# Kernel tuning notes

Measured on AMD Instinct MI355X. Metric: run time of the kernel, lower is better.

The kernel has to match this reference:

```python
import jax, jax.numpy as jnp
import numpy as np

N = 50000
E = 800000
IN_DIM = 128
OUT_DIM = 128
EDGE_DIM = 3
H = 4
HD = OUT_DIM // H  # 32
SCALE = HD ** -0.5


def setup_inputs() -> dict:
    key = jax.random.key(0)
    ks = jax.random.split(key, 10)
    x = jax.random.normal(ks[0], (N, IN_DIM), dtype=jnp.float32)
    edge_index = jax.random.randint(ks[1], (2, E), 0, N, dtype=jnp.int64)
    edge_attr = jax.random.normal(ks[2], (E, EDGE_DIM), dtype=jnp.float32)
    s = 1.0 / np.sqrt(IN_DIM)
    Wq = jax.random.normal(ks[3], (IN_DIM, H * HD), dtype=jnp.float32) * s
    Wk = jax.random.normal(ks[4], (IN_DIM, H * HD), dtype=jnp.float32) * s
    Wv = jax.random.normal(ks[5], (IN_DIM, H * HD), dtype=jnp.float32) * s
    We = jax.random.normal(ks[6], (EDGE_DIM, H), dtype=jnp.float32) * (1.0 / np.sqrt(EDGE_DIM))
    Wo = jax.random.normal(ks[7], (H * HD, OUT_DIM), dtype=jnp.float32) * (1.0 / np.sqrt(H * HD))
    bo = jnp.zeros((OUT_DIM,), dtype=jnp.float32)
    Wm = jax.random.normal(ks[8], (IN_DIM + OUT_DIM, OUT_DIM), dtype=jnp.float32) * (1.0 / np.sqrt(IN_DIM + OUT_DIM))
    bm = jnp.zeros((OUT_DIM,), dtype=jnp.float32)
    return {"x": x, "edge_index": edge_index, "edge_attr": edge_attr,
            "Wq": Wq, "Wk": Wk, "Wv": Wv, "We": We, "Wo": Wo, "bo": bo,
            "Wm": Wm, "bm": bm}


def reference(x, edge_index, edge_attr, Wq, Wk, Wv, We, Wo, bo, Wm, bm):
    n = x.shape[0]
    src = edge_index[0]
    dst = edge_index[1]
    Q = (x @ Wq).reshape(n, H, HD)
    K = (x @ Wk).reshape(n, H, HD)
    V = (x @ Wv).reshape(n, H, HD)
    edge_bias = edge_attr @ We                                  # [E, H]
    attn = jnp.sum(Q[dst] * K[src], axis=-1) * SCALE + edge_bias  # [E, H]
    attn = jnp.where(attn >= 0, attn, 0.2 * attn)               # leaky_relu(0.2)
    # NOTE: original uses a single GLOBAL max over all edges/heads for stability
    attn_exp = jnp.exp(attn - jnp.max(attn))
    attn_sum = jax.ops.segment_sum(attn_exp, dst, num_segments=n)  # [N, H]
    attn_norm = attn_exp / jnp.maximum(attn_sum[dst], 1e-12)
    # dropout disabled (eval mode)
    weighted_V = V[src] * attn_norm[:, :, None]                 # [E, H, HD]
    agg = jax.ops.segment_sum(weighted_V, dst, num_segments=n)  # [N, H, HD]
    agg = agg.reshape(n, H * HD) @ Wo + bo                      # [N, OUT]
    h = jnp.concatenate([x, agg], axis=1) @ Wm + bm
    return jax.nn.relu(h)
```

## Files before the change

kernel.cpp:

```cpp
#include <hip/hip_runtime.h>
#include <hip/hip_bf16.h>
#include <math.h>

#define NN 50000
#define NE 800000
#define DIM 128
#define NH 4
#define HD 32
#define EH (NE * NH)
#define ATTN_SCALE 0.17677669529663687f
#define MTILE 64
#define GEMM_BLOCKS 782
#define NBKT 98
#define PTS 2048
#define PBLKS 391
#define HBLKS 104

typedef unsigned int uint;
typedef unsigned short ushort;
typedef __attribute__((ext_vector_type(8))) short short8;
typedef __attribute__((ext_vector_type(4))) float f32x4;

__device__ inline ushort f2bf(float f) {
    __hip_bfloat16 h = __float2bfloat16(f);
    return *(ushort*)&h;
}
__device__ inline float bflo(uint u) { return __uint_as_float(u << 16); }
__device__ inline float bfhi(uint u) { return __uint_as_float(u & 0xffff0000u); }

__global__ __launch_bounds__(256) void prep_x_kernel(
    const float* __restrict__ x, ushort* __restrict__ xb)
{
    const int i = blockIdx.x * 256 + threadIdx.x;
    const float4 v = ((const float4*)x)[i];
    ushort4 o;
    o.x = f2bf(v.x); o.y = f2bf(v.y); o.z = f2bf(v.z); o.w = f2bf(v.w);
    ((ushort4*)xb)[i] = o;
}

__global__ __launch_bounds__(128) void prep_wx_kernel(
    const float* __restrict__ Wo, const float* __restrict__ Wm,
    float* __restrict__ Wx)
{
    const int r = blockIdx.x, j = threadIdx.x;
    float acc = 0.f;
    for (int t = 0; t < 128; ++t)
        acc = fmaf(Wo[r * 128 + t], Wm[(128 + t) * 128 + j], acc);
    Wx[r * 128 + j] = acc;
}

__global__ __launch_bounds__(128) void prep_bias_kernel(
    const float* __restrict__ bo, const float* __restrict__ bm,
    const float* __restrict__ Wm, float* __restrict__ bprime)
{
    const int j = threadIdx.x;
    float acc = bm[j];
    for (int t = 0; t < 128; ++t)
        acc = fmaf(bo[t], Wm[(128 + t) * 128 + j], acc);
    bprime[j] = acc;
}

__global__ __launch_bounds__(256) void pack_qkv_kernel(
    const float* __restrict__ Wq, const float* __restrict__ Wk,
    const float* __restrict__ Wv, short* __restrict__ Bp)
{
    const int idx = blockIdx.x * 256 + threadIdx.x;
    const int j = idx & 7, lane = (idx >> 3) & 63;
    const int rest = idx >> 9;
    const int nt = rest % 24, kc = rest / 24;
    const int k = kc * 32 + (lane >> 4) * 8 + j;
    const int n = nt * 16 + (lane & 15);
    const float* W = (n < 128) ? Wq : (n < 256 ? Wk : Wv);
    Bp[idx] = (short)f2bf(W[k * 128 + (n & 127)]);
}

__global__ __launch_bounds__(256) void pack_out_kernel(
    const float* __restrict__ Wm, const float* __restrict__ Wx,
    short* __restrict__ Bp)
{
    const int idx = blockIdx.x * 256 + threadIdx.x;
    const int j = idx & 7, lane = (idx >> 3) & 63;
    const int rest = idx >> 9;
    const int nt = rest & 7, kc = rest >> 3;
    const int k = kc * 32 + (lane >> 4) * 8 + j;
    const int n = nt * 16 + (lane & 15);
    const float v = (k < 128) ? Wm[k * 128 + n] : Wx[(k - 128) * 128 + n];
    Bp[idx] = (short)f2bf(v);
}

__global__ __launch_bounds__(128) void bkt_zero_kernel(int* __restrict__ bkt_cnt)
{
    if (threadIdx.x < 128) bkt_cnt[threadIdx.x] = 0;
}

__global__ __launch_bounds__(256) void bkt_hist_kernel(
    const int* __restrict__ dst, int* __restrict__ bkt_cnt)
{
    __shared__ int c[NBKT];
    const int tid = threadIdx.x;
    if (tid < NBKT) c[tid] = 0;
    __syncthreads();
    for (int e = blockIdx.x * 256 + tid; e < NE; e += HBLKS * 256)
        atomicAdd(&c[dst[e] >> 9], 1);
    __syncthreads();
    if (tid < NBKT && c[tid]) atomicAdd(&bkt_cnt[tid], c[tid]);
}

__global__ void bkt_scan_kernel(const int* __restrict__ bkt_cnt,
                                int* __restrict__ bkt_base,
                                int* __restrict__ bkt_cursor,
                                int* __restrict__ rowptr)
{
    if (threadIdx.x == 0) {
        int run = 0;
        for (int b = 0; b < NBKT; ++b) {
            bkt_base[b] = run;
            bkt_cursor[b] = run;
            run += bkt_cnt[b];
        }
        bkt_base[NBKT] = run;
        rowptr[NN] = run;
    }
}

__global__ __launch_bounds__(256) void partition_kernel(
    const int* __restrict__ src, const int* __restrict__ dst,
    const float* __restrict__ edge_attr, const float* __restrict__ We,
    int* __restrict__ bkt_cursor,
    int* __restrict__ psrc, int* __restrict__ pdst, float* __restrict__ peb)
{
    __shared__ int cnt[NBKT], rbase[NBKT], cnt2[NBKT];
    const int tid = threadIdx.x;
    if (tid < NBKT) cnt[tid] = 0;
    __syncthreads();
    const int e0 = blockIdx.x * PTS;
    #pragma unroll
    for (int it = 0; it < 8; ++it) {
        const int e = e0 + it * 256 + tid;
        if (e < NE) atomicAdd(&cnt[dst[e] >> 9], 1);
    }
    __syncthreads();
    if (tid < NBKT) {
        rbase[tid] = cnt[tid] ? atomicAdd(&bkt_cursor[tid], cnt[tid]) : 0;
        cnt2[tid] = 0;
    }
    __syncthreads();
    #pragma unroll
    for (int it = 0; it < 8; ++it) {
        const int e = e0 + it * 256 + tid;
        if (e < NE) {
            const int d = dst[e];
            const int b = d >> 9;
            const int r = atomicAdd(&cnt2[b], 1);
            const int pos = rbase[b] + r;
            psrc[pos] = src[e];
            pdst[pos] = d;
            const float a0 = edge_attr[e * 3 + 0];
            const float a1 = edge_attr[e * 3 + 1];
            const float a2 = edge_attr[e * 3 + 2];
            float4 eb;
            eb.x = a0 * We[0] + a1 * We[4] + a2 * We[8];
            eb.y = a0 * We[1] + a1 * We[5] + a2 * We[9];
            eb.z = a0 * We[2] + a1 * We[6] + a2 * We[10];
            eb.w = a0 * We[3] + a1 * We[7] + a2 * We[11];
            *(float4*)(peb + (size_t)pos * 4) = eb;
        }
    }
}

__global__ __launch_bounds__(256) void bucket_csr_kernel(
    const int* __restrict__ bkt_base,
    const int* __restrict__ psrc, const int* __restrict__ pdst,
    const float* __restrict__ peb,
    int* __restrict__ rowptr,
    int* __restrict__ srcp, float* __restrict__ eb_csr)
{
    __shared__ int cnt[512];
    __shared__ int pre[512];
    __shared__ int sc[256];
    const int tid = threadIdx.x;
    const int b = blockIdx.x;
    const int base = bkt_base[b];
    const int n = bkt_base[b + 1] - base;
    const int node0 = b << 9;

    cnt[tid] = 0; cnt[tid + 256] = 0;
    __syncthreads();
    for (int i = base + tid; i < base + n; i += 256)
        atomicAdd(&cnt[pdst[i] - node0], 1);
    __syncthreads();

    const int pair = cnt[2 * tid] + cnt[2 * tid + 1];
    sc[tid] = pair;
    __syncthreads();
    for (int off = 1; off < 256; off <<= 1) {
        const int v = (tid >= off) ? sc[tid - off] : 0;
        __syncthreads();
        sc[tid] += v;
        __syncthreads();
    }
    const int ex = sc[tid] - pair;
    pre[2 * tid] = base + ex;
    pre[2 * tid + 1] = base + ex + cnt[2 * tid];
    __syncthreads();

    for (int l = tid; l < 512; l += 256) {
        const int g = node0 + l;
        if (g < NN) rowptr[g] = pre[l];
    }
    __syncthreads();

    for (int i = base + tid; i < base + n; i += 256) {
        const int d = pdst[i];
        const int pos = atomicAdd(&pre[d - node0], 1);
        srcp[pos] = psrc[i];
        *(float4*)(eb_csr + (size_t)pos * 4) =
            *(const float4*)(peb + (size_t)i * 4);
    }
}

__global__ __launch_bounds__(256) void qkv_mfma_kernel(
    const ushort* __restrict__ xb, const short* __restrict__ Bp,
    ushort* __restrict__ Qb, ushort* __restrict__ Kb, ushort* __restrict__ Vb)
{
    const int wave = threadIdx.x >> 6;
    const int lane = threadIdx.x & 63;
    const int m = lane & 15, quad = lane >> 4;
    const int row0w = blockIdx.x * MTILE + wave * 16;
    const int arow = row0w + m;
    const bool rowok = arow < NN;

    short8 a[4];
    #pragma unroll
    for (int kc = 0; kc < 4; ++kc)
        a[kc] = rowok ? *(const short8*)(xb + (size_t)arow * 128 + kc * 32 + quad * 8)
                      : (short8)(0);

    const int NT = 24;
    for (int nt = 0; nt < NT; nt += 2) {
        f32x4 acc0 = {0.f, 0.f, 0.f, 0.f}, acc1 = {0.f, 0.f, 0.f, 0.f};
        #pragma unroll
        for (int kc = 0; kc < 4; ++kc) {
            const short8 b0 = *(const short8*)(Bp + ((size_t)(kc * NT + nt) * 64 + lane) * 8);
            const short8 b1 = *(const short8*)(Bp + ((size_t)(kc * NT + nt + 1) * 64 + lane) * 8);
            acc0 = __builtin_amdgcn_mfma_f32_16x16x32_bf16(a[kc], b0, acc0, 0, 0, 0);
            acc1 = __builtin_amdgcn_mfma_f32_16x16x32_bf16(a[kc], b1, acc1, 0, 0, 0);
        }
        #pragma unroll
        for (int t = 0; t < 2; ++t) {
            const f32x4 acc = t ? acc1 : acc0;
            const int c = (nt + t) * 16 + m;
            ushort* dstp_ = (c < 128) ? Qb : (c < 256 ? Kb : Vb);
            const int lc = c & 127;
            #pragma unroll
            for (int g = 0; g < 4; ++g) {
                const int r = row0w + quad * 4 + g;
                if (r < NN) dstp_[(size_t)r * 128 + lc] = f2bf(acc[g]);
            }
        }
    }
}

__global__ __launch_bounds__(256) void out_mfma_kernel(
    const ushort* __restrict__ xb, const ushort* __restrict__ aggb,
    const short* __restrict__ Bp, const float* __restrict__ bprime,
    float* __restrict__ out)
{
    const int wave = threadIdx.x >> 6;
    const int lane = threadIdx.x & 63;
    const int m = lane & 15, quad = lane >> 4;
    const int row0w = blockIdx.x * MTILE + wave * 16;
    const int arow = row0w + m;
    const bool rowok = arow < NN;

    short8 a[8];
    #pragma unroll
    for (int kc = 0; kc < 4; ++kc)
        a[kc] = rowok ? *(const short8*)(xb + (size_t)arow * 128 + kc * 32 + quad * 8)
                      : (short8)(0);
    #pragma unroll
    for (int kc = 0; kc < 4; ++kc)
        a[4 + kc] = rowok ? *(const short8*)(aggb + (size_t)arow * 128 + kc * 32 + quad * 8)
                          : (short8)(0);

    const int NT = 8;
    for (int nt = 0; nt < NT; nt += 2) {
        f32x4 acc0 = {0.f, 0.f, 0.f, 0.f}, acc1 = {0.f, 0.f, 0.f, 0.f};
        #pragma unroll
        for (int kc = 0; kc < 8; ++kc) {
            const short8 b0 = *(const short8*)(Bp + ((size_t)(kc * NT + nt) * 64 + lane) * 8);
            const short8 b1 = *(const short8*)(Bp + ((size_t)(kc * NT + nt + 1) * 64 + lane) * 8);
            acc0 = __builtin_amdgcn_mfma_f32_16x16x32_bf16(a[kc], b0, acc0, 0, 0, 0);
            acc1 = __builtin_amdgcn_mfma_f32_16x16x32_bf16(a[kc], b1, acc1, 0, 0, 0);
        }
        #pragma unroll
        for (int t = 0; t < 2; ++t) {
            const f32x4 acc = t ? acc1 : acc0;
            const int c = (nt + t) * 16 + m;
            const float bb = bprime[c];
            #pragma unroll
            for (int g = 0; g < 4; ++g) {
                const int r = row0w + quad * 4 + g;
                if (r < NN) out[(size_t)r * 128 + c] = fmaxf(acc[g] + bb, 0.f);
            }
        }
    }
}

__global__ __launch_bounds__(256) void attn_agg_kernel(
    const ushort* __restrict__ Qb, const ushort* __restrict__ Kb,
    const ushort* __restrict__ Vb,
    const int* __restrict__ rowptr, const int* __restrict__ srcp,
    const float* __restrict__ eb_csr, ushort* __restrict__ aggb)
{
    const int tid = threadIdx.x;
    const int d = blockIdx.x * 4 + (tid >> 6);
    const int lane = tid & 63;
    const int g = lane >> 4;
    const int t = lane & 15;
    const int h = t >> 2;
    const int begin = rowptr[d];
    const int end   = rowptr[d + 1];

    const uint4 uq = *(const uint4*)(Qb + (size_t)d * DIM + 8 * t);
    float q0 = bflo(uq.x), q1 = bfhi(uq.x);
    float q2 = bflo(uq.y), q3 = bfhi(uq.y);
    float q4 = bflo(uq.z), q5 = bfhi(uq.z);
    float q6 = bflo(uq.w), q7 = bfhi(uq.w);

    float ss = 0.f;
    float a0 = 0.f, a1 = 0.f, a2 = 0.f, a3 = 0.f;
    float a4 = 0.f, a5 = 0.f, a6 = 0.f, a7 = 0.f;

    if (begin < end) {
        const int last = end - 1;
        const ushort* kbase = Kb + 8 * t;
        const ushort* vbase = Vb + 8 * t;

        int e0 = begin + g;      e0 = (e0 > last) ? last : e0;
        int e1 = begin + 4 + g;  e1 = (e1 > last) ? last : e1;
        int e2 = begin + 8 + g;  e2 = (e2 > last) ? last : e2;
        int   sA = srcp[e0];  float ebA = eb_csr[(size_t)e0 * 4 + h];
        int   sB = srcp[e1];  float ebB = eb_csr[(size_t)e1 * 4 + h];
        int   sC = srcp[e2];  float ebC = eb_csr[(size_t)e2 * 4 + h];
        uint4 ukA = *(const uint4*)(kbase + (size_t)sA * DIM);
        uint4 uvA = *(const uint4*)(vbase + (size_t)sA * DIM);
        uint4 ukB = *(const uint4*)(kbase + (size_t)sB * DIM);
        uint4 uvB = *(const uint4*)(vbase + (size_t)sB * DIM);

        for (int p = begin; p < end; p += 4) {
            const uint4 ukC = *(const uint4*)(kbase + (size_t)sC * DIM);
            const uint4 uvC = *(const uint4*)(vbase + (size_t)sC * DIM);
            int e3 = p + 12 + g; e3 = (e3 > last) ? last : e3;
            const int   sD  = srcp[e3];
            const float ebD = eb_csr[(size_t)e3 * 4 + h];

            const bool ok = (p + g) < end;
            float da = q0 * bflo(ukA.x);
            float db = q1 * bfhi(ukA.x);
            da = fmaf(q2, bflo(ukA.y), da);
            db = fmaf(q3, bfhi(ukA.y), db);
            da = fmaf(q4, bflo(ukA.z), da);
            db = fmaf(q5, bfhi(ukA.z), db);
            da = fmaf(q6, bflo(ukA.w), da);
            db = fmaf(q7, bfhi(ukA.w), db);
            float part = da + db;
            part += __shfl_xor(part, 1);
            part += __shfl_xor(part, 2);

            float a = fmaf(part, ATTN_SCALE, ebA);
            a = (a >= 0.f) ? a : 0.2f * a;
            const float w = ok ? __expf(a) : 0.f;

            ss += w;
            a0 = fmaf(w, bflo(uvA.x), a0);
            a1 = fmaf(w, bfhi(uvA.x), a1);
            a2 = fmaf(w, bflo(uvA.y), a2);
            a3 = fmaf(w, bfhi(uvA.y), a3);
            a4 = fmaf(w, bflo(uvA.z), a4);
            a5 = fmaf(w, bfhi(uvA.z), a5);
            a6 = fmaf(w, bflo(uvA.w), a6);
            a7 = fmaf(w, bfhi(uvA.w), a7);

            ukA = ukB; uvA = uvB; ebA = ebB;
            ukB = ukC; uvB = uvC; ebB = ebC;
            sC = sD;   ebC = ebD;
        }
    }

    ss += __shfl_xor(ss, 16);
    ss += __shfl_xor(ss, 32);
    a0 += __shfl_xor(a0, 16); a0 += __shfl_xor(a0, 32);
    a1 += __shfl_xor(a1, 16); a1 += __shfl_xor(a1, 32);
    a2 += __shfl_xor(a2, 16); a2 += __shfl_xor(a2, 32);
    a3 += __shfl_xor(a3, 16); a3 += __shfl_xor(a3, 32);
    a4 += __shfl_xor(a4, 16); a4 += __shfl_xor(a4, 32);
    a5 += __shfl_xor(a5, 16); a5 += __shfl_xor(a5, 32);
    a6 += __shfl_xor(a6, 16); a6 += __shfl_xor(a6, 32);
    a7 += __shfl_xor(a7, 16); a7 += __shfl_xor(a7, 32);

    if (g == 0) {
        const float inv = 1.f / fmaxf(ss, 1e-12f);
        uint4 o;
        o.x = (uint)f2bf(a0 * inv) | ((uint)f2bf(a1 * inv) << 16);
        o.y = (uint)f2bf(a2 * inv) | ((uint)f2bf(a3 * inv) << 16);
        o.z = (uint)f2bf(a4 * inv) | ((uint)f2bf(a5 * inv) << 16);
        o.w = (uint)f2bf(a6 * inv) | ((uint)f2bf(a7 * inv) << 16);
        *(uint4*)(aggb + (size_t)d * DIM + 8 * t) = o;
    }
}

extern "C" void kernel_launch(void* const* d_in, const int* in_sizes, int n_in,
                              void* d_out, int out_size, void* d_ws, size_t ws_size,
                              hipStream_t stream)
{
    const float* x         = (const float*)d_in[0];
    const int*   edge_idx  = (const int*)d_in[1];
    const float* edge_attr = (const float*)d_in[2];
    const float* Wq        = (const float*)d_in[3];
    const float* Wk        = (const float*)d_in[4];
    const float* Wv        = (const float*)d_in[5];
    const float* We        = (const float*)d_in[6];
    const float* Wo        = (const float*)d_in[7];
    const float* bo        = (const float*)d_in[8];
    const float* Wm        = (const float*)d_in[9];
    const float* bm        = (const float*)d_in[10];
    float* out = (float*)d_out;

    const int* src = edge_idx;
    const int* dst = edge_idx + NE;

    ushort* xb   = (ushort*)d_ws;
    ushort* Qb   = xb + (size_t)NN * DIM;
    ushort* Kb   = Qb + (size_t)NN * DIM;
    ushort* Vb   = Kb + (size_t)NN * DIM;
    ushort* aggb = Vb + (size_t)NN * DIM;
    int*   psrc     = (int*)(aggb + (size_t)NN * DIM);
    int*   pdst     = psrc + NE;
    float* peb      = (float*)(pdst + NE);
    float* eb_csr   = peb + (size_t)EH;
    float* Wx       = eb_csr + (size_t)EH;
    float* bprime   = Wx + 16384;
    short* BpQKV    = (short*)(bprime + 128);
    short* BpOut    = BpQKV + 49152;
    int*   rowptr   = (int*)(BpOut + 32768);
    int*   srcp     = rowptr + 50048;
    int*   bkt_cnt    = srcp + NE;
    int*   bkt_base   = bkt_cnt + 128;
    int*   bkt_cursor = bkt_base + 128;

    prep_x_kernel<<<(NN * DIM / 4) / 256, 256, 0, stream>>>(x, xb);
    prep_wx_kernel<<<128, 128, 0, stream>>>(Wo, Wm, Wx);
    prep_bias_kernel<<<1, 128, 0, stream>>>(bo, bm, Wm, bprime);
    pack_qkv_kernel<<<192, 256, 0, stream>>>(Wq, Wk, Wv, BpQKV);
    pack_out_kernel<<<128, 256, 0, stream>>>(Wm, Wx, BpOut);

    bkt_zero_kernel<<<1, 128, 0, stream>>>(bkt_cnt);
    bkt_hist_kernel<<<HBLKS, 256, 0, stream>>>(dst, bkt_cnt);
    bkt_scan_kernel<<<1, 64, 0, stream>>>(bkt_cnt, bkt_base, bkt_cursor, rowptr);
    partition_kernel<<<PBLKS, 256, 0, stream>>>(src, dst, edge_attr, We,
                                                bkt_cursor, psrc, pdst, peb);
    bucket_csr_kernel<<<NBKT, 256, 0, stream>>>(bkt_base, psrc, pdst, peb,
                                                rowptr, srcp, eb_csr);

    qkv_mfma_kernel<<<GEMM_BLOCKS, 256, 0, stream>>>(xb, BpQKV, Qb, Kb, Vb);
    attn_agg_kernel<<<NN / 4, 256, 0, stream>>>(Qb, Kb, Vb, rowptr, srcp,
                                                eb_csr, aggb);
    out_mfma_kernel<<<GEMM_BLOCKS, 256, 0, stream>>>(xb, aggb, BpOut, bprime, out);
}
```

Before: 299.0 us.

## Fuse small prep launches and process two edge groups per attention iteration

Two tiny setup kernels are folded into others: the bucket-counter zeroing moves into prep_x_kernel, and the bias fold shares a launch with the Wx fold through an extra block. The attention aggregation loop now handles 8 edges per iteration in two independent X/Y accumulator sets. It issues both K/V gathers up front each iteration and prefetches the next indices one step ahead, replacing the earlier rotating three-deep register pipeline. The goal is fewer launches and more independent memory requests in flight per wave, at the cost of more registers and a shallower prefetch of K/V data.

```diff
diff --git a/kernel.cpp b/kernel.cpp
--- a/kernel.cpp
+++ b/kernel.cpp
@@ -29,8 +29,10 @@
 __device__ inline float bfhi(uint u) { return __uint_as_float(u & 0xffff0000u); }
 
 __global__ __launch_bounds__(256) void prep_x_kernel(
-    const float* __restrict__ x, ushort* __restrict__ xb)
-{
+    const float* __restrict__ x, ushort* __restrict__ xb,
+    int* __restrict__ bkt_cnt)
+{
+    if (blockIdx.x == 0 && threadIdx.x < 128) bkt_cnt[threadIdx.x] = 0;
     const int i = blockIdx.x * 256 + threadIdx.x;
     const float4 v = ((const float4*)x)[i];
     ushort4 o;
@@ -38,26 +40,23 @@
     ((ushort4*)xb)[i] = o;
 }
 
-__global__ __launch_bounds__(128) void prep_wx_kernel(
+__global__ __launch_bounds__(128) void prep_wxb_kernel(
     const float* __restrict__ Wo, const float* __restrict__ Wm,
-    float* __restrict__ Wx)
+    const float* __restrict__ bo, const float* __restrict__ bm,
+    float* __restrict__ Wx, float* __restrict__ bprime)
 {
     const int r = blockIdx.x, j = threadIdx.x;
-    float acc = 0.f;
-    for (int t = 0; t < 128; ++t)
-        acc = fmaf(Wo[r * 128 + t], Wm[(128 + t) * 128 + j], acc);
-    Wx[r * 128 + j] = acc;
-}
-
-__global__ __launch_bounds__(128) void prep_bias_kernel(
-    const float* __restrict__ bo, const float* __restrict__ bm,
-    const float* __restrict__ Wm, float* __restrict__ bprime)
-{
-    const int j = threadIdx.x;
-    float acc = bm[j];
-    for (int t = 0; t < 128; ++t)
-        acc = fmaf(bo[t], Wm[(128 + t) * 128 + j], acc);
-    bprime[j] = acc;
+    if (r < 128) {
+        float acc = 0.f;
+        for (int t = 0; t < 128; ++t)
+            acc = fmaf(Wo[r * 128 + t], Wm[(128 + t) * 128 + j], acc);
+        Wx[r * 128 + j] = acc;
+    } else {
+        float acc = bm[j];
+        for (int t = 0; t < 128; ++t)
+            acc = fmaf(bo[t], Wm[(128 + t) * 128 + j], acc);
+        bprime[j] = acc;
+    }
 }
 
 __global__ __launch_bounds__(256) void pack_qkv_kernel(
@@ -86,11 +85,6 @@
     const int n = nt * 16 + (lane & 15);
     const float v = (k < 128) ? Wm[k * 128 + n] : Wx[(k - 128) * 128 + n];
     Bp[idx] = (short)f2bf(v);
-}
-
-__global__ __launch_bounds__(128) void bkt_zero_kernel(int* __restrict__ bkt_cnt)
-{
-    if (threadIdx.x < 128) bkt_cnt[threadIdx.x] = 0;
 }
 
 __global__ __launch_bounds__(256) void bkt_hist_kernel(
@@ -323,70 +317,100 @@
     const int end   = rowptr[d + 1];
 
     const uint4 uq = *(const uint4*)(Qb + (size_t)d * DIM + 8 * t);
-    float q0 = bflo(uq.x), q1 = bfhi(uq.x);
-    float q2 = bflo(uq.y), q3 = bfhi(uq.y);
-    float q4 = bflo(uq.z), q5 = bfhi(uq.z);
-    float q6 = bflo(uq.w), q7 = bfhi(uq.w);
-
-    float ss = 0.f;
-    float a0 = 0.f, a1 = 0.f, a2 = 0.f, a3 = 0.f;
-    float a4 = 0.f, a5 = 0.f, a6 = 0.f, a7 = 0.f;
+    const float q0 = bflo(uq.x), q1 = bfhi(uq.x);
+    const float q2 = bflo(uq.y), q3 = bfhi(uq.y);
+    const float q4 = bflo(uq.z), q5 = bfhi(uq.z);
+    const float q6 = bflo(uq.w), q7 = bfhi(uq.w);
+
+    float ssX = 0.f, x0 = 0.f, x1 = 0.f, x2 = 0.f, x3 = 0.f;
+    float               x4 = 0.f, x5 = 0.f, x6 = 0.f, x7 = 0.f;
+    float ssY = 0.f, y0 = 0.f, y1 = 0.f, y2 = 0.f, y3 = 0.f;
+    float               y4 = 0.f, y5 = 0.f, y6 = 0.f, y7 = 0.f;
 
     if (begin < end) {
         const int last = end - 1;
         const ushort* kbase = Kb + 8 * t;
         const ushort* vbase = Vb + 8 * t;
 
-        int e0 = begin + g;      e0 = (e0 > last) ? last : e0;
-        int e1 = begin + 4 + g;  e1 = (e1 > last) ? last : e1;
-        int e2 = begin + 8 + g;  e2 = (e2 > last) ? last : e2;
-        int   sA = srcp[e0];  float ebA = eb_csr[(size_t)e0 * 4 + h];
-        int   sB = srcp[e1];  float ebB = eb_csr[(size_t)e1 * 4 + h];
-        int   sC = srcp[e2];  float ebC = eb_csr[(size_t)e2 * 4 + h];
-        uint4 ukA = *(const uint4*)(kbase + (size_t)sA * DIM);
-        uint4 uvA = *(const uint4*)(vbase + (size_t)sA * DIM);
-        uint4 ukB = *(const uint4*)(kbase + (size_t)sB * DIM);
-        uint4 uvB = *(const uint4*)(vbase + (size_t)sB * DIM);
-
-        for (int p = begin; p < end; p += 4) {
-            const uint4 ukC = *(const uint4*)(kbase + (size_t)sC * DIM);
-            const uint4 uvC = *(const uint4*)(vbase + (size_t)sC * DIM);
-            int e3 = p + 12 + g; e3 = (e3 > last) ? last : e3;
-            const int   sD  = srcp[e3];
-            const float ebD = eb_csr[(size_t)e3 * 4 + h];
-
-            const bool ok = (p + g) < end;
-            float da = q0 * bflo(ukA.x);
-            float db = q1 * bfhi(ukA.x);
-            da = fmaf(q2, bflo(ukA.y), da);
-            db = fmaf(q3, bfhi(ukA.y), db);
-            da = fmaf(q4, bflo(ukA.z), da);
-            db = fmaf(q5, bfhi(ukA.z), db);
-            da = fmaf(q6, bflo(ukA.w), da);
-            db = fmaf(q7, bfhi(ukA.w), db);
-            float part = da + db;
-            part += __shfl_xor(part, 1);
-            part += __shfl_xor(part, 2);
-
-            float a = fmaf(part, ATTN_SCALE, ebA);
-            a = (a >= 0.f) ? a : 0.2f * a;
-            const float w = ok ? __expf(a) : 0.f;
-
-            ss += w;
-            a0 = fmaf(w, bflo(uvA.x), a0);
-            a1 = fmaf(w, bfhi(uvA.x), a1);
-            a2 = fmaf(w, bflo(uvA.y), a2);
-            a3 = fmaf(w, bfhi(uvA.y), a3);
-            a4 = fmaf(w, bflo(uvA.z), a4);
-            a5 = fmaf(w, bfhi(uvA.z), a5);
-            a6 = fmaf(w, bflo(uvA.w), a6);
-            a7 = fmaf(w, bfhi(uvA.w), a7);
-
-            ukA = ukB; uvA = uvB; ebA = ebB;
-            ukB = ukC; uvB = uvC; ebB = ebC;
-            sC = sD;   ebC = ebD;
-        }
-    }
+        int eX = begin + g;      eX = (eX > last) ? last : eX;
+        int eY = begin + 4 + g;  eY = (eY > last) ? last : eY;
+        int   sX  = srcp[eX];
+        int   sY  = srcp[eY];
+        float ebX = eb_csr[(size_t)eX * 4 + h];
+        float ebY = eb_csr[(size_t)eY * 4 + h];
+
+        for (int p = begin; p < end; p += 8) {
+            int eXn = p + 8 + g;   eXn = (eXn > last) ? last : eXn;
+            int eYn = p + 12 + g;  eYn = (eYn > last) ? last : eYn;
+            const int   sXn  = srcp[eXn];
+            const int   sYn  = srcp[eYn];
+            const float ebXn = eb_csr[(size_t)eXn * 4 + h];
+            const float ebYn = eb_csr[(size_t)eYn * 4 + h];
+
+            const uint4 ukX = *(const uint4*)(kbase + (size_t)sX * DIM);
+            const uint4 uvX = *(const uint4*)(vbase + (size_t)sX * DIM);
+            const uint4 ukY = *(const uint4*)(kbase + (size_t)sY * DIM);
+            const uint4 uvY = *(const uint4*)(vbase + (size_t)sY * DIM);
+
+            {
+                const bool ok = (p + g) < end;
+                float da = q0 * bflo(ukX.x);
+                float db = q1 * bfhi(ukX.x);
+                da = fmaf(q2, bflo(ukX.y), da);
+                db = fmaf(q3, bfhi(ukX.y), db);
+                da = fmaf(q4, bflo(ukX.z), da);
+                db = fmaf(q5, bfhi(ukX.z), db);
+                da = fmaf(q6, bflo(ukX.w), da);
+                db = fmaf(q7, bfhi(ukX.w), db);
+                float part = da + db;
+                part += __shfl_xor(part, 1);
+                part += __shfl_xor(part, 2);
+                float a = fmaf(part, ATTN_SCALE, ebX);
+                a = (a >= 0.f) ? a : 0.2f * a;
+                const float w = ok ? __expf(a) : 0.f;
+                ssX += w;
+                x0 = fmaf(w, bflo(uvX.x), x0);
+                x1 = fmaf(w, bfhi(uvX.x), x1);
+                x2 = fmaf(w, bflo(uvX.y), x2);
+                x3 = fmaf(w, bfhi(uvX.y), x3);
+                x4 = fmaf(w, bflo(uvX.z), x4);
+                x5 = fmaf(w, bfhi(uvX.z), x5);
+                x6 = fmaf(w, bflo(uvX.w), x6);
+                x7 = fmaf(w, bfhi(uvX.w), x7);
+            }
+            {
+                const bool ok = (p + 4 + g) < end;
+                float da = q0 * bflo(ukY.x);
+                float db = q1 * bfhi(ukY.x);
+                da = fmaf(q2, bflo(ukY.y), da);
+                db = fmaf(q3, bfhi(ukY.y), db);
+                da = fmaf(q4, bflo(ukY.z), da);
+                db = fmaf(q5, bfhi(ukY.z), db);
+                da = fmaf(q6, bflo(ukY.w), da);
+                db = fmaf(q7, bfhi(ukY.w), db);
+                float part = da + db;
+                part += __shfl_xor(part, 1);
+                part += __shfl_xor(part, 2);
+                float a = fmaf(part, ATTN_SCALE, ebY);
+                a = (a >= 0.f) ? a : 0.2f * a;
+                const float w = ok ? __expf(a) : 0.f;
+                ssY += w;
+                y0 = fmaf(w, bflo(uvY.x), y0);
+                y1 = fmaf(w, bfhi(uvY.x), y1);
+                y2 = fmaf(w, bflo(uvY.y), y2);
+                y3 = fmaf(w, bfhi(uvY.y), y3);
+                y4 = fmaf(w, bflo(uvY.z), y4);
+                y5 = fmaf(w, bfhi(uvY.z), y5);
+                y6 = fmaf(w, bflo(uvY.w), y6);
+                y7 = fmaf(w, bfhi(uvY.w), y7);
+            }
+            sX = sXn; sY = sYn; ebX = ebXn; ebY = ebYn;
+        }
+    }
+
+    float ss = ssX + ssY;
+    float a0 = x0 + y0, a1 = x1 + y1, a2 = x2 + y2, a3 = x3 + y3;
+    float a4 = x4 + y4, a5 = x5 + y5, a6 = x6 + y6, a7 = x7 + y7;
 
     ss += __shfl_xor(ss, 16);
     ss += __shfl_xor(ss, 32);
@@ -449,13 +473,11 @@
     int*   bkt_base   = bkt_cnt + 128;
     int*   bkt_cursor = bkt_base + 128;
 
-    prep_x_kernel<<<(NN * DIM / 4) / 256, 256, 0, stream>>>(x, xb);
-    prep_wx_kernel<<<128, 128, 0, stream>>>(Wo, Wm, Wx);
-    prep_bias_kernel<<<1, 128, 0, stream>>>(bo, bm, Wm, bprime);
+    prep_x_kernel<<<(NN * DIM / 4) / 256, 256, 0, stream>>>(x, xb, bkt_cnt);
+    prep_wxb_kernel<<<129, 128, 0, stream>>>(Wo, Wm, bo, bm, Wx, bprime);
     pack_qkv_kernel<<<192, 256, 0, stream>>>(Wq, Wk, Wv, BpQKV);
     pack_out_kernel<<<128, 256, 0, stream>>>(Wm, Wx, BpOut);
 
-    bkt_zero_kernel<<<1, 128, 0, stream>>>(bkt_cnt);
     bkt_hist_kernel<<<HBLKS, 256, 0, stream>>>(dst, bkt_cnt);
     bkt_scan_kernel<<<1, 64, 0, stream>>>(bkt_cnt, bkt_base, bkt_cursor, rowptr);
     partition_kernel<<<PBLKS, 256, 0, stream>>>(src, dst, edge_attr, We,
```

Result: faster. 278.6 us (-6.8%).
